# Kernel optimization log

Measured on AMD Instinct MI355X. Metric: run time of the kernel, lower is better.

The kernel has to match this reference:

```python
import jax, jax.numpy as jnp
import numpy as np

PATCH = 3      # forward default patch_size
ALPHA = 1.0    # forward default alpha
# scale_factor = 1 -> F.interpolate is the identity


def setup_inputs() -> dict:
    key = jax.random.key(0)
    x_l = jax.random.normal(key, (16, 1, 1536, 1536), dtype=jnp.float32)
    return {"x_l": x_l}


def reference(x_l):
    # x_l: [N, 1, H, W]
    N, C, H, W = x_l.shape
    p = PATCH
    pad = p // 2
    # zero-padded input, matching F.unfold's implicit zero padding
    xp = jnp.pad(x_l, ((0, 0), (0, 0), (pad, pad), (pad, pad)))
    # gather the p*p shifted views -> [N, p*p, H, W] (equivalent to F.unfold for C=1;
    # softmax + weighted sum over dim 1 is permutation-invariant over the patch axis)
    local = jnp.stack(
        [xp[:, 0, i:i + H, j:j + W] for i in range(p) for j in range(p)],
        axis=1,
    )
    # local_difference = local_l - x_l**2  (broadcast over the patch dim)
    diff = local - x_l[:, 0][:, None, :, :] ** 2
    corr = jax.nn.softmax(-diff / ALPHA, axis=1)
    # softmax-weighted local average -> [N, 1, H, W]
    return jnp.sum(corr * local, axis=1, keepdims=True)
```

## Files before the change

kernel.cpp:

```cpp
#include <hip/hip_runtime.h>
#include <math.h>

#define IMG_W 1536
#define IMG_H 1536
#define NIMG  16
#define RPB 8
#define NROWS (RPB + 2)

typedef float f32x4 __attribute__((ext_vector_type(4)));

__global__ __launch_bounds__(128)
void WeightedAverage_55551107006568_kernel(const float* __restrict__ x,
                                           float* __restrict__ out) {
    const int g  = blockIdx.x * 128 + threadIdx.x;
    const int w0 = g << 2;
    const int h0 = blockIdx.y * RPB;
    const size_t plane = (size_t)blockIdx.z * ((size_t)IMG_H * IMG_W);
    const float* xp = x + plane;
    float* op = out + plane;

    f32x4 m[NROWS];
    float hl[NROWS], hr[NROWS];
    const bool lok = (w0 > 0);
    const bool rok = (w0 + 4 < IMG_W);
#pragma unroll
    for (int i = 0; i < NROWS; ++i) {
        const int r = h0 - 1 + i;
        f32x4 mm = {0.f, 0.f, 0.f, 0.f};
        float hlv = 0.f, hrv = 0.f;
        if (r >= 0 && r < IMG_H) {
            const float* rp = xp + (size_t)r * IMG_W + w0;
            mm = *(const f32x4*)rp;
            if (lok) hlv = rp[-1];
            if (rok) hrv = rp[4];
        }
        m[i] = mm; hl[i] = hlv; hr[i] = hrv;
    }
    __builtin_amdgcn_sched_barrier(0);

    float hE[3][4], hVE[3][4];
#pragma unroll
    for (int i = 0; i < NROWS; ++i) {
        const int r = h0 - 1 + i;
        const int s = i % 3;
        if (r < 0 || r >= IMG_H) {
#pragma unroll
            for (int p = 0; p < 4; ++p) { hE[s][p] = 3.f; hVE[s][p] = 0.f; }
        } else {
            const f32x4 mm = m[i];
            const float eL = __expf(-hl[i]), vL = hl[i] * eL;
            const float e0 = __expf(-mm.x),  v0 = mm.x * e0;
            const float e1 = __expf(-mm.y),  v1 = mm.y * e1;
            const float e2 = __expf(-mm.z),  v2 = mm.z * e2;
            const float e3 = __expf(-mm.w),  v3 = mm.w * e3;
            const float eR = __expf(-hr[i]), vR = hr[i] * eR;
            hE[s][0] = eL + e0 + e1;  hVE[s][0] = vL + v0 + v1;
            hE[s][1] = e0 + e1 + e2;  hVE[s][1] = v0 + v1 + v2;
            hE[s][2] = e1 + e2 + e3;  hVE[s][2] = v1 + v2 + v3;
            hE[s][3] = e2 + e3 + eR;  hVE[s][3] = v2 + v3 + vR;
        }

        if (i >= 2) {
            const int ro = h0 + i - 2;
            f32x4 o;
#pragma unroll
            for (int p = 0; p < 4; ++p) {
                const float den = hE[0][p] + hE[1][p] + hE[2][p];
                const float num = hVE[0][p] + hVE[1][p] + hVE[2][p];
                o[p] = __fdividef(num, den);
            }
            __builtin_nontemporal_store(o, (f32x4*)(op + (size_t)ro * IMG_W + w0));
        }
    }
}

extern "C" void kernel_launch(void* const* d_in, const int* in_sizes, int n_in,
                              void* d_out, int out_size, void* d_ws, size_t ws_size,
                              hipStream_t stream) {
    const float* x = (const float*)d_in[0];
    float* out = (float*)d_out;
    dim3 grid(IMG_W / (128 * 4), IMG_H / RPB, NIMG);
    dim3 block(128, 1, 1);
    WeightedAverage_55551107006568_kernel<<<grid, block, 0, stream>>>(x, out);
}
```

Measured before the change: 254.5 us.

## Software-pipeline row loads with prefetch window and taller row blocks

Raises rows per block from 8 to 32, so fewer halo rows are reloaded per block. Replaces the up-front load of all rows with a rolling prefetch of 6 rows ahead, interleaved with the exp/sum compute. Out-of-range rows and halo columns now use clamped, branch-free loads with select-based zeroing. In exchange the grid has 4x fewer blocks, which lowers occupancy and parallelism for this memory-bound stencil.

Result: slower. 263.0 us (+3.3%).

```diff
diff --git a/kernel.cpp b/kernel.cpp
--- a/kernel.cpp
+++ b/kernel.cpp
@@ -4,8 +4,9 @@
 #define IMG_W 1536
 #define IMG_H 1536
 #define NIMG  16
-#define RPB 8
+#define RPB   32
 #define NROWS (RPB + 2)
+#define PF    6
 
 typedef float f32x4 __attribute__((ext_vector_type(4)));
 
@@ -19,46 +20,52 @@
     const float* xp = x + plane;
     float* op = out + plane;
 
+    const bool lok = (w0 > 0);
+    const bool rok = (w0 + 4 < IMG_W);
+    const int offL = lok ? -4 : 0;
+    const int offR = rok ? 16 : 0;
+
     f32x4 m[NROWS];
     float hl[NROWS], hr[NROWS];
-    const bool lok = (w0 > 0);
-    const bool rok = (w0 + 4 < IMG_W);
+
+    auto issue = [&](int i) {
+        const int r  = h0 - 1 + i;
+        const int rc = r < 0 ? 0 : (r >= IMG_H ? IMG_H - 1 : r);
+        const float* rp = xp + (size_t)rc * IMG_W + w0;
+        m[i]  = *(const f32x4*)rp;
+        hl[i] = *(const float*)((const char*)rp + offL);
+        hr[i] = *(const float*)((const char*)rp + offR);
+    };
+
 #pragma unroll
-    for (int i = 0; i < NROWS; ++i) {
-        const int r = h0 - 1 + i;
-        f32x4 mm = {0.f, 0.f, 0.f, 0.f};
-        float hlv = 0.f, hrv = 0.f;
-        if (r >= 0 && r < IMG_H) {
-            const float* rp = xp + (size_t)r * IMG_W + w0;
-            mm = *(const f32x4*)rp;
-            if (lok) hlv = rp[-1];
-            if (rok) hrv = rp[4];
-        }
-        m[i] = mm; hl[i] = hlv; hr[i] = hrv;
-    }
+    for (int i = 0; i < PF; ++i) issue(i);
     __builtin_amdgcn_sched_barrier(0);
 
     float hE[3][4], hVE[3][4];
 #pragma unroll
     for (int i = 0; i < NROWS; ++i) {
-        const int r = h0 - 1 + i;
+        if (i + PF < NROWS) issue(i + PF);
+        __builtin_amdgcn_sched_barrier(0);
+
+        const int r  = h0 - 1 + i;
+        const bool rv = (r >= 0) && (r < IMG_H);
         const int s = i % 3;
-        if (r < 0 || r >= IMG_H) {
-#pragma unroll
-            for (int p = 0; p < 4; ++p) { hE[s][p] = 3.f; hVE[s][p] = 0.f; }
-        } else {
-            const f32x4 mm = m[i];
-            const float eL = __expf(-hl[i]), vL = hl[i] * eL;
-            const float e0 = __expf(-mm.x),  v0 = mm.x * e0;
-            const float e1 = __expf(-mm.y),  v1 = mm.y * e1;
-            const float e2 = __expf(-mm.z),  v2 = mm.z * e2;
-            const float e3 = __expf(-mm.w),  v3 = mm.w * e3;
-            const float eR = __expf(-hr[i]), vR = hr[i] * eR;
-            hE[s][0] = eL + e0 + e1;  hVE[s][0] = vL + v0 + v1;
-            hE[s][1] = e0 + e1 + e2;  hVE[s][1] = v0 + v1 + v2;
-            hE[s][2] = e1 + e2 + e3;  hVE[s][2] = v1 + v2 + v3;
-            hE[s][3] = e2 + e3 + eR;  hVE[s][3] = v2 + v3 + vR;
-        }
+
+        f32x4 mm = m[i];
+        float hlv = (rv && lok) ? hl[i] : 0.f;
+        float hrv = (rv && rok) ? hr[i] : 0.f;
+        if (!rv) mm = (f32x4){0.f, 0.f, 0.f, 0.f};
+
+        const float eL = __expf(-hlv),  vL = hlv * eL;
+        const float e0 = __expf(-mm.x), v0 = mm.x * e0;
+        const float e1 = __expf(-mm.y), v1 = mm.y * e1;
+        const float e2 = __expf(-mm.z), v2 = mm.z * e2;
+        const float e3 = __expf(-mm.w), v3 = mm.w * e3;
+        const float eR = __expf(-hrv),  vR = hrv * eR;
+        hE[s][0] = eL + e0 + e1;  hVE[s][0] = vL + v0 + v1;
+        hE[s][1] = e0 + e1 + e2;  hVE[s][1] = v0 + v1 + v2;
+        hE[s][2] = e1 + e2 + e3;  hVE[s][2] = v1 + v2 + v3;
+        hE[s][3] = e2 + e3 + eR;  hVE[s][3] = v2 + v3 + vR;
 
         if (i >= 2) {
             const int ro = h0 + i - 2;
```

## Compute one output row per block with three-row loads instead of rolling window

Applied to the files above, without the earlier changes.

Each block now produces a single output row instead of eight. Every thread loads its three neighbouring rows and halo values directly, with clamped addresses and zero-masking at the borders. The goal is many more independent, short-lived blocks and fewer live registers, which should give better latency hiding and occupancy; a launch-bounds hint of 8 blocks is added for the same reason. The cost is that each input row is read three times and its exponentials are recomputed three times, where the old rolling window reused them across rows.

New measurement: 267.8 us. 5.2% more time.

```diff
diff --git a/kernel.cpp b/kernel.cpp
--- a/kernel.cpp
+++ b/kernel.cpp
@@ -4,74 +4,77 @@
 #define IMG_W 1536
 #define IMG_H 1536
 #define NIMG  16
-#define RPB 8
-#define NROWS (RPB + 2)
 
 typedef float f32x4 __attribute__((ext_vector_type(4)));
 
-__global__ __launch_bounds__(128)
+__global__ __launch_bounds__(128, 8)
 void WeightedAverage_55551107006568_kernel(const float* __restrict__ x,
                                            float* __restrict__ out) {
-    const int g  = blockIdx.x * 128 + threadIdx.x;
-    const int w0 = g << 2;
-    const int h0 = blockIdx.y * RPB;
+    const int tid = threadIdx.x;
+    const int w0  = ((blockIdx.x << 7) + tid) << 2;
+    const int h   = blockIdx.y;
     const size_t plane = (size_t)blockIdx.z * ((size_t)IMG_H * IMG_W);
-    const float* xp = x + plane;
+    const float* xp = x + plane + w0;
     float* op = out + plane;
 
-    f32x4 m[NROWS];
-    float hl[NROWS], hr[NROWS];
     const bool lok = (w0 > 0);
     const bool rok = (w0 + 4 < IMG_W);
-#pragma unroll
-    for (int i = 0; i < NROWS; ++i) {
-        const int r = h0 - 1 + i;
-        f32x4 mm = {0.f, 0.f, 0.f, 0.f};
-        float hlv = 0.f, hrv = 0.f;
-        if (r >= 0 && r < IMG_H) {
-            const float* rp = xp + (size_t)r * IMG_W + w0;
-            mm = *(const f32x4*)rp;
-            if (lok) hlv = rp[-1];
-            if (rok) hrv = rp[4];
-        }
-        m[i] = mm; hl[i] = hlv; hr[i] = hrv;
-    }
+    const int offL = lok ? -4 : 0;
+    const int offR = rok ? 16 : 0;
+
+    const bool tv = (h > 0);
+    const bool bv = (h < IMG_H - 1);
+    const int hm = tv ? h - 1 : 0;
+    const int hp = bv ? h + 1 : IMG_H - 1;
+
+    const float* r0 = xp + (size_t)hm * IMG_W;
+    const float* r1 = xp + (size_t)h  * IMG_W;
+    const float* r2 = xp + (size_t)hp * IMG_W;
+
+    f32x4 m0 = *(const f32x4*)r0;
+    float a0 = *(const float*)((const char*)r0 + offL);
+    float b0 = *(const float*)((const char*)r0 + offR);
+    f32x4 m1 = *(const f32x4*)r1;
+    float a1 = *(const float*)((const char*)r1 + offL);
+    float b1 = *(const float*)((const char*)r1 + offR);
+    f32x4 m2 = *(const f32x4*)r2;
+    float a2 = *(const float*)((const char*)r2 + offL);
+    float b2 = *(const float*)((const char*)r2 + offR);
     __builtin_amdgcn_sched_barrier(0);
 
-    float hE[3][4], hVE[3][4];
+    if (!tv) { m0 = (f32x4){0.f, 0.f, 0.f, 0.f}; a0 = 0.f; b0 = 0.f; }
+    if (!bv) { m2 = (f32x4){0.f, 0.f, 0.f, 0.f}; a2 = 0.f; b2 = 0.f; }
+    if (!lok) { a0 = 0.f; a1 = 0.f; a2 = 0.f; }
+    if (!rok) { b0 = 0.f; b1 = 0.f; b2 = 0.f; }
+
+    f32x4 den = {0.f, 0.f, 0.f, 0.f};
+    f32x4 num = {0.f, 0.f, 0.f, 0.f};
+    {
+        const f32x4 mr[3] = {m0, m1, m2};
+        const float ha[3] = {a0, a1, a2};
+        const float hb[3] = {b0, b1, b2};
 #pragma unroll
-    for (int i = 0; i < NROWS; ++i) {
-        const int r = h0 - 1 + i;
-        const int s = i % 3;
-        if (r < 0 || r >= IMG_H) {
-#pragma unroll
-            for (int p = 0; p < 4; ++p) { hE[s][p] = 3.f; hVE[s][p] = 0.f; }
-        } else {
-            const f32x4 mm = m[i];
-            const float eL = __expf(-hl[i]), vL = hl[i] * eL;
+        for (int i = 0; i < 3; ++i) {
+            const f32x4 mm = mr[i];
+            const float eL = __expf(-ha[i]), vL = ha[i] * eL;
             const float e0 = __expf(-mm.x),  v0 = mm.x * e0;
             const float e1 = __expf(-mm.y),  v1 = mm.y * e1;
             const float e2 = __expf(-mm.z),  v2 = mm.z * e2;
             const float e3 = __expf(-mm.w),  v3 = mm.w * e3;
-            const float eR = __expf(-hr[i]), vR = hr[i] * eR;
-            hE[s][0] = eL + e0 + e1;  hVE[s][0] = vL + v0 + v1;
-            hE[s][1] = e0 + e1 + e2;  hVE[s][1] = v0 + v1 + v2;
-            hE[s][2] = e1 + e2 + e3;  hVE[s][2] = v1 + v2 + v3;
-            hE[s][3] = e2 + e3 + eR;  hVE[s][3] = v2 + v3 + vR;
-        }
-
-        if (i >= 2) {
-            const int ro = h0 + i - 2;
-            f32x4 o;
-#pragma unroll
-            for (int p = 0; p < 4; ++p) {
-                const float den = hE[0][p] + hE[1][p] + hE[2][p];
-                const float num = hVE[0][p] + hVE[1][p] + hVE[2][p];
-                o[p] = __fdividef(num, den);
-            }
-            __builtin_nontemporal_store(o, (f32x4*)(op + (size_t)ro * IMG_W + w0));
+            const float eR = __expf(-hb[i]), vR = hb[i] * eR;
+            den.x += eL + e0 + e1;  num.x += vL + v0 + v1;
+            den.y += e0 + e1 + e2;  num.y += v0 + v1 + v2;
+            den.z += e1 + e2 + e3;  num.z += v1 + v2 + v3;
+            den.w += e2 + e3 + eR;  num.w += v2 + v3 + vR;
         }
     }
+
+    f32x4 o;
+    o.x = __fdividef(num.x, den.x);
+    o.y = __fdividef(num.y, den.y);
+    o.z = __fdividef(num.z, den.z);
+    o.w = __fdividef(num.w, den.w);
+    __builtin_nontemporal_store(o, (f32x4*)(op + (size_t)h * IMG_W + w0));
 }
 
 extern "C" void kernel_launch(void* const* d_in, const int* in_sizes, int n_in,
@@ -79,7 +82,7 @@
                               hipStream_t stream) {
     const float* x = (const float*)d_in[0];
     float* out = (float*)d_out;
-    dim3 grid(IMG_W / (128 * 4), IMG_H / RPB, NIMG);
+    dim3 grid(IMG_W / (128 * 4), IMG_H, NIMG);
     dim3 block(128, 1, 1);
     WeightedAverage_55551107006568_kernel<<<grid, block, 0, stream>>>(x, out);
 }
```

## Use wave shuffles for halo, XCD-aware 1D grid, and smaller row tiles

Applied to the files above, without the earlier changes.

Each thread no longer loads its own left and right halo scalars. Neighbouring exp and weighted values are exchanged with wave shuffles, and only the edge lanes (0 and 63) load halo elements. The launch becomes a flat 1D grid in which each XCD is assigned two whole images, which improves L2 locality of the vertical overlap. Rows per block drop from 8 to 4, and launch bounds ask for higher occupancy. The aim is to cut redundant, uncoalesced global loads, at the cost of extra cross-lane operations and a larger vertical halo overhead per output row.

Measured after the change: 256.7 us. Within noise of the previous version (+0.9%).

```diff
diff --git a/kernel.cpp b/kernel.cpp
--- a/kernel.cpp
+++ b/kernel.cpp
@@ -4,73 +4,98 @@
 #define IMG_W 1536
 #define IMG_H 1536
 #define NIMG  16
-#define RPB 8
-#define NROWS (RPB + 2)
+#define RPB   4
+#define NRW   (RPB + 2)
 
 typedef float f32x4 __attribute__((ext_vector_type(4)));
 
-__global__ __launch_bounds__(128)
+__global__ __launch_bounds__(128, 6)
 void WeightedAverage_55551107006568_kernel(const float* __restrict__ x,
                                            float* __restrict__ out) {
-    const int g  = blockIdx.x * 128 + threadIdx.x;
-    const int w0 = g << 2;
-    const int h0 = blockIdx.y * RPB;
-    const size_t plane = (size_t)blockIdx.z * ((size_t)IMG_H * IMG_W);
-    const float* xp = x + plane;
-    float* op = out + plane;
+    const int bid   = blockIdx.x;
+    const int xcd   = bid & 7;
+    const int chunk = bid >> 3;
+    const int z     = (xcd << 1) + (chunk / 1152);
+    const int rem   = chunk % 1152;
+    const int yb    = rem / 3;
+    const int xb    = rem - yb * 3;
+    const int h0    = yb << 2;
+    const int w0    = ((xb << 7) + threadIdx.x) << 2;
 
-    f32x4 m[NROWS];
-    float hl[NROWS], hr[NROWS];
-    const bool lok = (w0 > 0);
-    const bool rok = (w0 + 4 < IMG_W);
+    const size_t plane = (size_t)z * ((size_t)IMG_H * IMG_W);
+    const float* xp = x + plane + w0;
+    float* op = out + plane + w0;
+
+    const int lane = threadIdx.x & 63;
+    const bool doL = (lane == 0)  && (w0 > 0);
+    const bool doR = (lane == 63) && (w0 + 4 < IMG_W);
+
+    int roff[NRW];
 #pragma unroll
-    for (int i = 0; i < NROWS; ++i) {
-        const int r = h0 - 1 + i;
-        f32x4 mm = {0.f, 0.f, 0.f, 0.f};
-        float hlv = 0.f, hrv = 0.f;
-        if (r >= 0 && r < IMG_H) {
-            const float* rp = xp + (size_t)r * IMG_W + w0;
-            mm = *(const f32x4*)rp;
-            if (lok) hlv = rp[-1];
-            if (rok) hrv = rp[4];
-        }
-        m[i] = mm; hl[i] = hlv; hr[i] = hrv;
+    for (int i = 0; i < NRW; ++i) {
+        int r = h0 - 1 + i;
+        r = r < 0 ? 0 : (r >= IMG_H ? IMG_H - 1 : r);
+        roff[i] = r * IMG_W;
+    }
+
+    f32x4 m[NRW];
+#pragma unroll
+    for (int i = 0; i < NRW; ++i) m[i] = *(const f32x4*)(xp + roff[i]);
+    float hl[NRW] = {0.f,0.f,0.f,0.f,0.f,0.f};
+    float hr[NRW] = {0.f,0.f,0.f,0.f,0.f,0.f};
+    if (doL) {
+#pragma unroll
+        for (int i = 0; i < NRW; ++i) hl[i] = xp[roff[i] - 1];
+    }
+    if (doR) {
+#pragma unroll
+        for (int i = 0; i < NRW; ++i) hr[i] = xp[roff[i] + 4];
     }
     __builtin_amdgcn_sched_barrier(0);
 
-    float hE[3][4], hVE[3][4];
+    if (h0 == 0) {
+        m[0] = (f32x4){0.f,0.f,0.f,0.f}; hl[0] = 0.f; hr[0] = 0.f;
+    }
+    if (h0 + NRW - 2 >= IMG_H) {
+        m[NRW-1] = (f32x4){0.f,0.f,0.f,0.f}; hl[NRW-1] = 0.f; hr[NRW-1] = 0.f;
+    }
+
+    f32x4 den[RPB], num[RPB];
 #pragma unroll
-    for (int i = 0; i < NROWS; ++i) {
-        const int r = h0 - 1 + i;
-        const int s = i % 3;
-        if (r < 0 || r >= IMG_H) {
+    for (int j = 0; j < RPB; ++j) {
+        den[j] = (f32x4){0.f,0.f,0.f,0.f};
+        num[j] = (f32x4){0.f,0.f,0.f,0.f};
+    }
 #pragma unroll
-            for (int p = 0; p < 4; ++p) { hE[s][p] = 3.f; hVE[s][p] = 0.f; }
-        } else {
-            const f32x4 mm = m[i];
-            const float eL = __expf(-hl[i]), vL = hl[i] * eL;
-            const float e0 = __expf(-mm.x),  v0 = mm.x * e0;
-            const float e1 = __expf(-mm.y),  v1 = mm.y * e1;
-            const float e2 = __expf(-mm.z),  v2 = mm.z * e2;
-            const float e3 = __expf(-mm.w),  v3 = mm.w * e3;
-            const float eR = __expf(-hr[i]), vR = hr[i] * eR;
-            hE[s][0] = eL + e0 + e1;  hVE[s][0] = vL + v0 + v1;
-            hE[s][1] = e0 + e1 + e2;  hVE[s][1] = v0 + v1 + v2;
-            hE[s][2] = e1 + e2 + e3;  hVE[s][2] = v1 + v2 + v3;
-            hE[s][3] = e2 + e3 + eR;  hVE[s][3] = v2 + v3 + vR;
-        }
+    for (int i = 0; i < NRW; ++i) {
+        const f32x4 mm = m[i];
+        const float e0 = __expf(-mm.x), v0 = mm.x * e0;
+        const float e1 = __expf(-mm.y), v1 = mm.y * e1;
+        const float e2 = __expf(-mm.z), v2 = mm.z * e2;
+        const float e3 = __expf(-mm.w), v3 = mm.w * e3;
+        const float elh = __expf(-hl[i]), vlh = hl[i] * elh;
+        const float erh = __expf(-hr[i]), vrh = hr[i] * erh;
+        const float e3s = __shfl_up(e3, 1),   v3s = __shfl_up(v3, 1);
+        const float e0s = __shfl_down(e0, 1), v0s = __shfl_down(v0, 1);
+        const float eL = (lane == 0)  ? elh : e3s;
+        const float vL = (lane == 0)  ? vlh : v3s;
+        const float eR = (lane == 63) ? erh : e0s;
+        const float vR = (lane == 63) ? vrh : v0s;
+        const f32x4 he = {eL + e0 + e1, e0 + e1 + e2, e1 + e2 + e3, e2 + e3 + eR};
+        const f32x4 hv = {vL + v0 + v1, v0 + v1 + v2, v1 + v2 + v3, v2 + v3 + vR};
+#pragma unroll
+        for (int j = 0; j < RPB; ++j)
+            if (j <= i && i <= j + 2) { den[j] += he; num[j] += hv; }
+    }
 
-        if (i >= 2) {
-            const int ro = h0 + i - 2;
-            f32x4 o;
 #pragma unroll
-            for (int p = 0; p < 4; ++p) {
-                const float den = hE[0][p] + hE[1][p] + hE[2][p];
-                const float num = hVE[0][p] + hVE[1][p] + hVE[2][p];
-                o[p] = __fdividef(num, den);
-            }
-            __builtin_nontemporal_store(o, (f32x4*)(op + (size_t)ro * IMG_W + w0));
-        }
+    for (int j = 0; j < RPB; ++j) {
+        f32x4 o;
+        o.x = __fdividef(num[j].x, den[j].x);
+        o.y = __fdividef(num[j].y, den[j].y);
+        o.z = __fdividef(num[j].z, den[j].z);
+        o.w = __fdividef(num[j].w, den[j].w);
+        __builtin_nontemporal_store(o, (f32x4*)(op + (size_t)(h0 + j) * IMG_W));
     }
 }
 
@@ -79,7 +104,7 @@
                               hipStream_t stream) {
     const float* x = (const float*)d_in[0];
     float* out = (float*)d_out;
-    dim3 grid(IMG_W / (128 * 4), IMG_H / RPB, NIMG);
+    dim3 grid(18432, 1, 1);
     dim3 block(128, 1, 1);
     WeightedAverage_55551107006568_kernel<<<grid, block, 0, stream>>>(x, out);
 }
```
